# Optimization experiments

Measured on AMD Instinct MI355X. Metric: run time of the kernel, lower is better.

The kernel has to match this reference:

```python
import jax, jax.numpy as jnp
import numpy as np

B, S, E, M = 128, 196, 768, 768

def setup_inputs() -> dict:
    key = jax.random.key(0)
    k1, k2, k3, k4, k5 = jax.random.split(key, 5)
    sent_emb = jax.random.normal(k1, (B, S, E), dtype=jnp.float32)
    # valid event spans: start in [0, S-6), end = start + len, len in [1,5]
    starts = jax.random.randint(k2, (B, 2), 0, S - 6)
    lens = jax.random.randint(k3, (B, 2), 1, 6)
    ends = starts + lens
    batch_e = jnp.stack([starts[:, 0], ends[:, 0], starts[:, 1], ends[:, 1]], axis=1).astype(jnp.int64)
    mlp_w = jax.random.normal(k4, (M, 2 * E), dtype=jnp.float32) * 0.02
    mlp_b = jnp.zeros((M,), dtype=jnp.float32)
    fk_w = jax.random.normal(k5, (M, S * E), dtype=jnp.float32) * 0.005
    fk_b = jnp.zeros((M,), dtype=jnp.float32)
    return {"sent_emb": sent_emb, "batch_e": batch_e, "mlp_w": mlp_w,
            "mlp_b": mlp_b, "fk_w": fk_w, "fk_b": fk_b, "batch_size": B}

def reference(sent_emb, batch_e, mlp_w, mlp_b, fk_w, fk_b, batch_size):
    b, s, e = sent_emb.shape
    # sent_process: flatten each sentence's [S,E] embeddings into one row [S*E]
    sent_emb_cat = sent_emb.reshape(b, s * e)  # [B, S*E]
    # extract_event: mean-pool over the two variable-length spans (vectorized via masks)
    pos = jnp.arange(s)  # [S]
    m1 = ((pos >= batch_e[:, 0:1]) & (pos < batch_e[:, 1:2])).astype(sent_emb.dtype)  # [B,S]
    m2 = ((pos >= batch_e[:, 2:3]) & (pos < batch_e[:, 3:4])).astype(sent_emb.dtype)
    e1 = jnp.einsum('bs,bse->be', m1, sent_emb) / jnp.sum(m1, axis=1, keepdims=True)
    e2 = jnp.einsum('bs,bse->be', m2, sent_emb) / jnp.sum(m2, axis=1, keepdims=True)
    event_pair = jnp.concatenate([e1, e2], axis=1)  # [B, 2E]
    pred = 0.9 * (event_pair @ mlp_w.T + mlp_b) + 0.1 * (sent_emb_cat @ fk_w.T + fk_b)
    return pred
```

## Files before the change

kernel.cpp:

```cpp
#include <hip/hip_runtime.h>
#include <hip/hip_bf16.h>

#define B_ 128
#define S_ 196
#define E_ 768
#define M_ 768
#define KTOT (S_*E_)
#define BK 256
#define SS_TOTAL (KTOT/BK)
#define KSPLIT 32
#define BN 48
#define MTN (M_/BN)
#define PITCH 528
#define ZC 4

typedef __bf16 bf16x8 __attribute__((ext_vector_type(8)));
typedef __bf16 bf16x4 __attribute__((ext_vector_type(4)));
typedef float  f32x4  __attribute__((ext_vector_type(4)));

__device__ inline bf16x8 cvt8(const float* __restrict__ p) {
    float4 a = *(const float4*)p;
    float4 b = *(const float4*)(p + 4);
    bf16x8 r;
    r[0] = (__bf16)a.x; r[1] = (__bf16)a.y; r[2] = (__bf16)a.z; r[3] = (__bf16)a.w;
    r[4] = (__bf16)b.x; r[5] = (__bf16)b.y; r[6] = (__bf16)b.z; r[7] = (__bf16)b.w;
    return r;
}

__global__ void prep(const float* __restrict__ mlp_b,
                     const float* __restrict__ fk_b,
                     const float* __restrict__ A,
                     const int* __restrict__ BE, int be_stride,
                     float* __restrict__ out,
                     float* __restrict__ EP,
                     __bf16* __restrict__ Apk) {
    const int bid = blockIdx.x;
    if (bid < 384) {
        int i = bid * 256 + threadIdx.x;
        int m = i % M_;
        out[i] = 0.9f * mlp_b[m] + 0.1f * fk_b[m];
    } else if (bid < 512) {
        int b = bid - 384;
        int s1 = BE[(b*4 + 0) * be_stride];
        int e1 = BE[(b*4 + 1) * be_stride];
        int s2 = BE[(b*4 + 2) * be_stride];
        int e2 = BE[(b*4 + 3) * be_stride];
        float inv1 = 1.0f / (float)(e1 - s1);
        float inv2 = 1.0f / (float)(e2 - s2);
        for (int c = threadIdx.x; c < E_; c += 256) {
            float sum1 = 0.f, sum2 = 0.f;
            for (int s = s1; s < e1; ++s) sum1 += A[((size_t)b * S_ + s) * E_ + c];
            for (int s = s2; s < e2; ++s) sum2 += A[((size_t)b * S_ + s) * E_ + c];
            EP[b * (2*E_) + c]       = sum1 * inv1;
            EP[b * (2*E_) + E_ + c]  = sum2 * inv2;
        }
    } else {
        const int nchunk = SS_TOTAL * 8 * 8 * 64;
        for (int c = (bid - 512) * 256 + threadIdx.x; c < nchunk; c += 3072 * 256) {
            int lane = c & 63;
            int kf   = (c >> 6) & 7;
            int bt   = (c >> 9) & 7;
            int ss   = c >> 12;
            int b = bt * 16 + (lane & 15);
            int k = ss * BK + kf * 32 + (lane >> 4) * 8;
            *(bf16x8*)(Apk + (size_t)c * 8) = cvt8(A + (size_t)b * KTOT + k);
        }
    }
}


#define LOAD_A(AREG, sl)                                                      \
    _Pragma("unroll")                                                         \
    for (int kf = 0; kf < 8; ++kf)                                            \
        AREG[kf] = *(const bf16x8*)(abase + (size_t)(sl) * 32768 + kf * 512);

#define LOAD_W(sl)                                                            \
    _Pragma("unroll")                                                         \
    for (int i = 0; i < 6; ++i)                                               \
        w[i] = *(const float4*)(wbase + (size_t)i * KTOT + (size_t)(sl) * BK);

#define WRITE_W(buf)                                                          \
    _Pragma("unroll")                                                         \
    for (int i = 0; i < 6; ++i) {                                             \
        bf16x4 h;                                                             \
        h[0] = (__bf16)w[i].x; h[1] = (__bf16)w[i].y;                         \
        h[2] = (__bf16)w[i].z; h[3] = (__bf16)w[i].w;                         \
        *(bf16x4*)(&Wlds[buf][0] + wb + i * PITCH) = h;                       \
    }

#define COMPUTE(AREG, buf)                                                    \
    _Pragma("unroll")                                                         \
    for (int kf = 0; kf < 8; ++kf) {                                          \
        _Pragma("unroll")                                                     \
        for (int n = 0; n < 3; ++n) {                                         \
            bf16x8 wf = *(const bf16x8*)(&Wlds[buf][0] +                      \
                        (n * 16 + r16) * PITCH + kf * 64 + kg * 16);          \
            acc[n] = __builtin_amdgcn_mfma_f32_16x16x32_bf16(AREG[kf], wf,    \
                                                             acc[n], 0, 0, 0);\
        }                                                                     \
    }

__global__ __launch_bounds__(512, 4) void fk_gemm(const __bf16* __restrict__ Apk,
                                                  const float* __restrict__ W,
                                                  float* __restrict__ partial) {
    __shared__ __align__(16) char Wlds[2][BN * PITCH];

    const int wg = blockIdx.x;
    const int mt = wg & (MTN - 1);
    const int kz = wg >> 4;
    const int ss0 = (SS_TOTAL * kz) / KSPLIT;
    const int SSN = (SS_TOTAL * (kz + 1)) / KSPLIT - ss0;

    const int tid = threadIdx.x;
    const int wv  = tid >> 6;
    const int lane = tid & 63;
    const int r16 = lane & 15;
    const int kg  = lane >> 4;

    const float*  wbase = W + (size_t)(mt * BN + wv * 6) * KTOT
                            + (size_t)ss0 * BK + lane * 4;
    const int     wb    = (wv * 6) * PITCH + lane * 8;
    const __bf16* abase = Apk + ((size_t)ss0 * 8 + wv) * 4096 + lane * 8;

    f32x4 acc[3] = {};
    float4 w[6];
    bf16x8 aA[8], aB[8];

    LOAD_W(0)
    WRITE_W(0)
    LOAD_A(aA, 0)
    LOAD_W(1)
    __syncthreads();

    int sl = 0;
    for (; sl + 1 < SSN; sl += 2) {
        LOAD_A(aB, sl + 1)
        COMPUTE(aA, 0)
        WRITE_W(1)
        const bool more2 = (sl + 2 < SSN);
        if (more2) { LOAD_W(sl + 2) }
        __syncthreads();
        if (more2) { LOAD_A(aA, sl + 2) }
        COMPUTE(aB, 1)
        if (more2) {
            WRITE_W(0)
            if (sl + 3 < SSN) { LOAD_W(sl + 3) }
            __syncthreads();
        }
    }
    if (SSN & 1) {
        COMPUTE(aA, 0)
    }

    float* pz = partial + (size_t)kz * (B_ * M_);
#pragma unroll
    for (int n = 0; n < 3; ++n) {
        const int m = mt * BN + n * 16 + r16;
#pragma unroll
        for (int r = 0; r < 4; ++r) {
            const int b = wv * 16 + kg * 4 + r;
            pz[(size_t)b * M_ + m] = acc[n][r];
        }
    }
}

__global__ __launch_bounds__(256) void post(const float* __restrict__ pp,
                                            const float* __restrict__ EP,
                                            const float* __restrict__ Wm,
                                            float* __restrict__ out) {
    const int bid = blockIdx.x;
    if (bid < 1536) {
        int t = bid * 256 + threadIdx.x;
        int i = t % (B_ * M_);
        int zc = t / (B_ * M_);
        float s = 0.f;
#pragma unroll
        for (int z = zc * (KSPLIT / ZC); z < (zc + 1) * (KSPLIT / ZC); ++z)
            s += pp[(size_t)z * (B_ * M_) + i];
        atomicAdd(out + i, 0.1f * s);
    } else {
        const int wid   = ((bid - 1536) * 256 + threadIdx.x) >> 6;
        const int lane  = threadIdx.x & 63;
        const int bt    = wid & 7;
        const int mt    = wid >> 3;
        const int row16 = lane & 15;
        const int kgrp  = lane >> 4;
        const float* Arow = EP + (size_t)(bt*16 + row16) * (2*E_);
        const float* Brow = Wm + (size_t)(mt*16 + row16) * (2*E_);
        f32x4 acc = {};
        for (int k0 = 0; k0 < 2*E_; k0 += 32) {
            bf16x8 af = cvt8(Arow + k0 + kgrp*8);
            bf16x8 bv = cvt8(Brow + k0 + kgrp*8);
            acc = __builtin_amdgcn_mfma_f32_16x16x32_bf16(af, bv, acc, 0, 0, 0);
        }
        const int m = mt*16 + row16;
#pragma unroll
        for (int r = 0; r < 4; ++r) {
            const int b = bt*16 + kgrp*4 + r;
            atomicAdd(out + b * M_ + m, 0.9f * acc[r]);
        }
    }
}

extern "C" void kernel_launch(void* const* d_in, const int* in_sizes, int n_in,
                              void* d_out, int out_size, void* d_ws, size_t ws_size,
                              hipStream_t stream) {
    const float* se    = (const float*)d_in[0];
    const int*   be    = (const int*)  d_in[1];
    const float* mlp_w = (const float*)d_in[2];
    const float* mlp_b = (const float*)d_in[3];
    const float* fk_w  = (const float*)d_in[4];
    const float* fk_b  = (const float*)d_in[5];
    float* out = (float*)d_out;
    float* ep  = (float*)d_ws;
    float* pp  = ep + (size_t)B_ * 2 * E_;
    __bf16* apk = (__bf16*)(pp + (size_t)KSPLIT * B_ * M_);

    const int be_stride = (in_sizes[1] == B_ * 4 * 2) ? 2 : 1;

    prep<<<3584, 256, 0, stream>>>(mlp_b, fk_b, se, be, be_stride, out, ep, apk);
    fk_gemm<<<MTN * KSPLIT, 512, 0, stream>>>(apk, fk_w, pp);
    post<<<1632, 256, 0, stream>>>(pp, ep, mlp_w, out);
}
```

Measured before the change: 172.5 us.

## Restructure fk GEMM into per-wave 128x32 tiles with swizzled LDS and 42-way K split

Rewrites the large split-K GEMM so each wave owns a 32-column slice of the weight and computes all 128 batch rows, holding 16 accumulators. Each wave keeps its own swizzled LDS weight buffer, so the kernel has no __syncthreads, and it streams the packed activations per k-fragment. The K split goes from 32 to 42 with 128-thread workgroups, and the grid index is remapped. The reduction kernel is resized to match. The goal is more reuse of each loaded weight fragment and no block-level barriers, in exchange for higher register pressure, more partial sums to reduce, and activations being reread by every wave.

```diff
diff --git a/kernel.cpp b/kernel.cpp
--- a/kernel.cpp
+++ b/kernel.cpp
@@ -8,11 +8,9 @@
 #define KTOT (S_*E_)
 #define BK 256
 #define SS_TOTAL (KTOT/BK)
-#define KSPLIT 32
-#define BN 48
-#define MTN (M_/BN)
-#define PITCH 528
-#define ZC 4
+#define KSPLIT 42
+#define SSN (SS_TOTAL/KSPLIT)
+#define ZC 6
 
 typedef __bf16 bf16x8 __attribute__((ext_vector_type(8)));
 typedef __bf16 bf16x4 __attribute__((ext_vector_type(4)));
@@ -69,97 +67,109 @@
 }
 
 
-#define LOAD_A(AREG, sl)                                                      \
+#define S_CHK(WR, j, sl)                                                      \
     _Pragma("unroll")                                                         \
-    for (int kf = 0; kf < 8; ++kf)                                            \
-        AREG[kf] = *(const bf16x8*)(abase + (size_t)(sl) * 32768 + kf * 512);
-
-#define LOAD_W(sl)                                                            \
+    for (int i = 0; i < 4; ++i)                                               \
+        WR[i] = *(const float4*)(wrow + (size_t)(4*(j)+i) * KTOT              \
+                                      + (size_t)(sl) * BK);
+
+#define W_CHK(WR, j)                                                          \
     _Pragma("unroll")                                                         \
-    for (int i = 0; i < 6; ++i)                                               \
-        w[i] = *(const float4*)(wbase + (size_t)i * KTOT + (size_t)(sl) * BK);
-
-#define WRITE_W(buf)                                                          \
+    for (int i = 0; i < 4; ++i) {                                             \
+        const int r = 4*(j)+i;                                                \
+        bf16x4 h;                                                             \
+        h[0] = (__bf16)WR[i].x; h[1] = (__bf16)WR[i].y;                       \
+        h[2] = (__bf16)WR[i].z; h[3] = (__bf16)WR[i].w;                       \
+        *(bf16x4*)(lds + r * 512 + ((lane * 8) ^ ((r & 7) << 4))) = h;        \
+    }
+
+#define LOAD_A(AREG, sl, kf)                                                  \
     _Pragma("unroll")                                                         \
-    for (int i = 0; i < 6; ++i) {                                             \
-        bf16x4 h;                                                             \
-        h[0] = (__bf16)w[i].x; h[1] = (__bf16)w[i].y;                         \
-        h[2] = (__bf16)w[i].z; h[3] = (__bf16)w[i].w;                         \
-        *(bf16x4*)(&Wlds[buf][0] + wb + i * PITCH) = h;                       \
-    }
-
-#define COMPUTE(AREG, buf)                                                    \
-    _Pragma("unroll")                                                         \
-    for (int kf = 0; kf < 8; ++kf) {                                          \
+    for (int bt = 0; bt < 8; ++bt)                                            \
+        AREG[bt] = *(const bf16x8*)(abase +                                   \
+            (((size_t)(ss0 + (sl)) * 8 + bt) * 8 + (kf)) * 512);
+
+#define CALC(AREG, kf)                                                        \
+    {                                                                         \
+        bf16x8 wf0 = *(const bf16x8*)(lds + (r16) * 512 +                     \
+                     (((kf) * 64 + kg * 16) ^ swz));                          \
+        bf16x8 wf1 = *(const bf16x8*)(lds + (16 + r16) * 512 +                \
+                     (((kf) * 64 + kg * 16) ^ swz));                          \
         _Pragma("unroll")                                                     \
-        for (int n = 0; n < 3; ++n) {                                         \
-            bf16x8 wf = *(const bf16x8*)(&Wlds[buf][0] +                      \
-                        (n * 16 + r16) * PITCH + kf * 64 + kg * 16);          \
-            acc[n] = __builtin_amdgcn_mfma_f32_16x16x32_bf16(AREG[kf], wf,    \
-                                                             acc[n], 0, 0, 0);\
+        for (int bt = 0; bt < 8; ++bt) {                                      \
+            acc[bt*2]   = __builtin_amdgcn_mfma_f32_16x16x32_bf16(AREG[bt],   \
+                              wf0, acc[bt*2],   0, 0, 0);                     \
+            acc[bt*2+1] = __builtin_amdgcn_mfma_f32_16x16x32_bf16(AREG[bt],   \
+                              wf1, acc[bt*2+1], 0, 0, 0);                     \
         }                                                                     \
     }
 
-__global__ __launch_bounds__(512, 4) void fk_gemm(const __bf16* __restrict__ Apk,
+__global__ __launch_bounds__(128, 2) void fk_gemm(const __bf16* __restrict__ Apk,
                                                   const float* __restrict__ W,
                                                   float* __restrict__ partial) {
-    __shared__ __align__(16) char Wlds[2][BN * PITCH];
-
-    const int wg = blockIdx.x;
-    const int mt = wg & (MTN - 1);
-    const int kz = wg >> 4;
-    const int ss0 = (SS_TOTAL * kz) / KSPLIT;
-    const int SSN = (SS_TOTAL * (kz + 1)) / KSPLIT - ss0;
-
-    const int tid = threadIdx.x;
-    const int wv  = tid >> 6;
-    const int lane = tid & 63;
-    const int r16 = lane & 15;
-    const int kg  = lane >> 4;
-
-    const float*  wbase = W + (size_t)(mt * BN + wv * 6) * KTOT
-                            + (size_t)ss0 * BK + lane * 4;
-    const int     wb    = (wv * 6) * PITCH + lane * 8;
-    const __bf16* abase = Apk + ((size_t)ss0 * 8 + wv) * 4096 + lane * 8;
-
-    f32x4 acc[3] = {};
-    float4 w[6];
-    bf16x8 aA[8], aB[8];
-
-    LOAD_W(0)
-    WRITE_W(0)
-    LOAD_A(aA, 0)
-    LOAD_W(1)
-    __syncthreads();
-
-    int sl = 0;
-    for (; sl + 1 < SSN; sl += 2) {
-        LOAD_A(aB, sl + 1)
-        COMPUTE(aA, 0)
-        WRITE_W(1)
-        const bool more2 = (sl + 2 < SSN);
-        if (more2) { LOAD_W(sl + 2) }
-        __syncthreads();
-        if (more2) { LOAD_A(aA, sl + 2) }
-        COMPUTE(aB, 1)
-        if (more2) {
-            WRITE_W(0)
-            if (sl + 3 < SSN) { LOAD_W(sl + 3) }
-            __syncthreads();
-        }
-    }
-    if (SSN & 1) {
-        COMPUTE(aA, 0)
+    __shared__ __align__(16) char Wlds[2][32 * 512];
+
+    const int wgid = blockIdx.x;
+    const int w    = (wgid & 7) * 63 + (wgid >> 3);
+    const int kz   = w / 12;
+    const int mtg  = w % 12;
+    const int wv   = threadIdx.x >> 6;
+    const int lane = threadIdx.x & 63;
+    const int r16  = lane & 15;
+    const int kg   = lane >> 4;
+    const int swz  = (r16 & 7) << 4;
+    const int mt32 = mtg * 2 + wv;
+    const int ss0  = kz * SSN;
+
+    char* lds = &Wlds[wv][0];
+
+    const float* wrow = W + (size_t)(mt32 * 32) * KTOT
+                          + (size_t)ss0 * BK + lane * 4;
+    const __bf16* abase = Apk + lane * 8;
+
+    f32x4 acc[16] = {};
+    float4 wA[4], wB[4], wC[4], wD[4];
+    bf16x8 aTA[8], aTB[8];
+
+    S_CHK(wA, 0, 0) S_CHK(wB, 1, 0) S_CHK(wC, 2, 0) S_CHK(wD, 3, 0)
+    W_CHK(wA, 0)    W_CHK(wB, 1)    W_CHK(wC, 2)    W_CHK(wD, 3)
+    S_CHK(wA, 4, 0) S_CHK(wB, 5, 0) S_CHK(wC, 6, 0) S_CHK(wD, 7, 0)
+    W_CHK(wA, 4)    W_CHK(wB, 5)    W_CHK(wC, 6)    W_CHK(wD, 7)
+
+    for (int sl = 0; sl < SSN; ++sl) {
+        const bool more = (sl + 1 < SSN);
+        if (more) { S_CHK(wA, 0, sl+1) S_CHK(wB, 1, sl+1)
+                    S_CHK(wC, 2, sl+1) S_CHK(wD, 3, sl+1) }
+
+        LOAD_A(aTA, sl, 0)
+#pragma unroll
+        for (int kp = 0; kp < 4; ++kp) {
+            LOAD_A(aTB, sl, 2*kp + 1)
+            CALC(aTA, 2*kp)
+            if (kp < 3) { LOAD_A(aTA, sl, 2*kp + 2) }
+            CALC(aTB, 2*kp + 1)
+        }
+
+        if (more) {
+            W_CHK(wA, 0) S_CHK(wA, 4, sl+1)
+            W_CHK(wB, 1) S_CHK(wB, 5, sl+1)
+            W_CHK(wC, 2) S_CHK(wC, 6, sl+1)
+            W_CHK(wD, 3) S_CHK(wD, 7, sl+1)
+            W_CHK(wA, 4) W_CHK(wB, 5) W_CHK(wC, 6) W_CHK(wD, 7)
+        }
     }
 
     float* pz = partial + (size_t)kz * (B_ * M_);
 #pragma unroll
-    for (int n = 0; n < 3; ++n) {
-        const int m = mt * BN + n * 16 + r16;
-#pragma unroll
-        for (int r = 0; r < 4; ++r) {
-            const int b = wv * 16 + kg * 4 + r;
-            pz[(size_t)b * M_ + m] = acc[n][r];
+    for (int bt = 0; bt < 8; ++bt) {
+#pragma unroll
+        for (int mi = 0; mi < 2; ++mi) {
+            const int m = mt32 * 32 + mi * 16 + r16;
+#pragma unroll
+            for (int r = 0; r < 4; ++r) {
+                const int b = bt * 16 + kg * 4 + r;
+                pz[(size_t)b * M_ + m] = acc[bt*2 + mi][r];
+            }
         }
     }
 }
@@ -169,7 +179,7 @@
                                             const float* __restrict__ Wm,
                                             float* __restrict__ out) {
     const int bid = blockIdx.x;
-    if (bid < 1536) {
+    if (bid < 2304) {
         int t = bid * 256 + threadIdx.x;
         int i = t % (B_ * M_);
         int zc = t / (B_ * M_);
@@ -179,7 +189,7 @@
             s += pp[(size_t)z * (B_ * M_) + i];
         atomicAdd(out + i, 0.1f * s);
     } else {
-        const int wid   = ((bid - 1536) * 256 + threadIdx.x) >> 6;
+        const int wid   = ((bid - 2304) * 256 + threadIdx.x) >> 6;
         const int lane  = threadIdx.x & 63;
         const int bt    = wid & 7;
         const int mt    = wid >> 3;
@@ -219,6 +229,6 @@
     const int be_stride = (in_sizes[1] == B_ * 4 * 2) ? 2 : 1;
 
     prep<<<3584, 256, 0, stream>>>(mlp_b, fk_b, se, be, be_stride, out, ep, apk);
-    fk_gemm<<<MTN * KSPLIT, 512, 0, stream>>>(apk, fk_w, pp);
-    post<<<1632, 256, 0, stream>>>(pp, ep, mlp_w, out);
-}
+    fk_gemm<<<12 * KSPLIT, 128, 0, stream>>>(apk, fk_w, pp);
+    post<<<2400, 256, 0, stream>>>(pp, ep, mlp_w, out);
+}
```

Result: slower. 287.0 us (+66.4%).
